# Kernel optimization log

Measured on AMD Instinct MI355X. Metric: run time of the kernel, lower is better.

## Reference

```python
import jax, jax.numpy as jnp
import numpy as np

K = 20          # neighbors per centroid
OUT_CH = 256    # out_channel
EPS = 1e-5      # batchnorm eps


def _bn(x, gamma, beta, axes):
    # batch-norm in training mode (batch statistics), per-channel on last axis
    mu = jnp.mean(x, axis=axes, keepdims=True)
    var = jnp.var(x, axis=axes, keepdims=True)
    return (x - mu) * jax.lax.rsqrt(var + EPS) * gamma + beta


def _forward(centroid, xyz, radius, dist,
             w_xyz, b_xyz, g0, be0, w1, g1, be1, w2, g2, be2):
    B, N, _ = xyz.shape
    M = centroid.shape[1]
    # --- sample_and_group: radius mask + index sort + gather ---
    ar = jnp.arange(N, dtype=jnp.int32)                       # [N]
    idx = jnp.where(dist > radius, N, ar[None, None, :])      # [B,M,N]
    idx = jnp.sort(idx, axis=-1)[:, :, :K]                    # [B,M,K] lowest in-radius indices
    first = idx[:, :, :1]
    idx = jnp.where(idx == N, first, idx)                     # pad with first neighbor
    pf = jax.vmap(lambda f, i: f[i])(xyz, idx)                # [B,M,K,3] gather
    # --- concat (points, neighbors, variance) -> 9 channels ---
    pts = jnp.broadcast_to(centroid[:, :, None, :], (B, M, K, 3))
    feat = jnp.concatenate([pts, pf, pf - pts], axis=-1)      # [B,M,K,9]
    # --- 1x1 conv2d + BN2d + GELU (exact erf, as torch nn.GELU) ---
    h = jnp.einsum('bmkc,oc->bmko', feat, w_xyz) + b_xyz      # [B,M,K,C/8]
    h = jax.nn.gelu(_bn(h, g0, be0, axes=(0, 1, 2)), approximate=False)
    # --- max over k neighbors ---
    h = jnp.max(h, axis=2)                                    # [B,M,C/8]
    # --- MLP: Conv1x1 (no bias) + BN1d + GELU, then Conv1x1 + BN1d ---
    h = jnp.einsum('bmc,oc->bmo', h, w1)
    h = jax.nn.gelu(_bn(h, g1, be1, axes=(0, 1)), approximate=False)
    h = jnp.einsum('bmc,oc->bmo', h, w2)
    h = _bn(h, g2, be2, axes=(0, 1))                          # [B,M,OUT_CH]
    return h


def setup_inputs() -> dict:
    key = jax.random.key(0)
    ks = jax.random.split(key, 10)
    B, M, N = 4, 2048, 8192
    c8, c4 = OUT_CH // 8, OUT_CH // 4
    return {
        'centroid': jax.random.uniform(ks[0], (B, M, 3), jnp.float32),
        'xyz': jax.random.uniform(ks[1], (B, N, 3), jnp.float32),
        'radius': jax.random.uniform(ks[2], (B, M, 1), jnp.float32),
        'dist': jax.random.uniform(ks[3], (B, M, N), jnp.float32),
        'w_xyz': jax.random.normal(ks[4], (c8, 9), jnp.float32) * 0.3,
        'b_xyz': jnp.zeros((c8,), jnp.float32),
        'g0': jnp.ones((c8,), jnp.float32),
        'be0': jnp.zeros((c8,), jnp.float32),
        'w1': jax.random.normal(ks[5], (c4, c8), jnp.float32) * 0.2,
        'g1': jnp.ones((c4,), jnp.float32),
        'be1': jnp.zeros((c4,), jnp.float32),
        'w2': jax.random.normal(ks[6], (OUT_CH, c4), jnp.float32) * 0.15,
        'g2': jnp.ones((OUT_CH,), jnp.float32),
        'be2': jnp.zeros((OUT_CH,), jnp.float32),
    }


def reference(centroid, xyz, radius, dist, w_xyz, b_xyz, g0, be0,
              w1, g1, be1, w2, g2, be2):
    return _forward(centroid, xyz, radius, dist, w_xyz, b_xyz, g0, be0,
                    w1, g1, be1, w2, g2, be2)
```

## Files before the change

### kernel.cpp

```cpp
#include <hip/hip_runtime.h>
#include <cstdint>
#include <cstddef>

#define K_NB   20
#define N_PTS  8192
#define C8     32
#define C4     64
#define COUT   256
#define EPSV   1e-5f
#define NROWS  8192
#define NBLK   1024
#define RPW    2
#define NP0    32
#define NP1    32
#define NP2    32

__device__ __forceinline__ float gelu_exact(float x) {
    return 0.5f * x * (1.0f + erff(x * 0.7071067811865476f));
}

__device__ __forceinline__ void grid_barrier(unsigned* __restrict__ arrive,
                                             unsigned* __restrict__ release,
                                             unsigned tag) {
    __syncthreads();
    if (blockIdx.x == 0) {
        for (int i = threadIdx.x; i < NBLK; i += 256) {
            if (i != 0)
                while (__hip_atomic_load(&arrive[i], __ATOMIC_RELAXED,
                                         __HIP_MEMORY_SCOPE_AGENT) != tag)
                    __builtin_amdgcn_s_sleep(1);
        }
        __syncthreads();
        if (threadIdx.x == 0)
            __hip_atomic_store(&release[tag], tag, __ATOMIC_RELEASE,
                               __HIP_MEMORY_SCOPE_AGENT);
    } else {
        if (threadIdx.x == 0) {
            __hip_atomic_store(&arrive[blockIdx.x], tag, __ATOMIC_RELEASE,
                               __HIP_MEMORY_SCOPE_AGENT);
            while (__hip_atomic_load(&release[tag], __ATOMIC_RELAXED,
                                     __HIP_MEMORY_SCOPE_AGENT) != tag)
                __builtin_amdgcn_s_sleep(1);
        }
        __syncthreads();
    }
}

__device__ __forceinline__ double agent_load(const double* p) {
    return __hip_atomic_load(p, __ATOMIC_RELAXED, __HIP_MEMORY_SCOPE_AGENT);
}

__device__ __forceinline__ int chunk_process(const float4* v, float rad, int base,
                                             int lane, int* __restrict__ idxp, int cnt) {
    #pragma unroll
    for (int s = 0; s < 4; s++) {
        unsigned mloc = (v[s].x <= rad ? 1u : 0u) | (v[s].y <= rad ? 2u : 0u)
                      | (v[s].z <= rad ? 4u : 0u) | (v[s].w <= rad ? 8u : 0u);
        uint64_t b0 = __ballot(mloc & 1u);
        uint64_t b1 = __ballot(mloc & 2u);
        uint64_t b2 = __ballot(mloc & 4u);
        uint64_t b3 = __ballot(mloc & 8u);
        uint64_t lt = (1ull << lane) - 1ull;
        int r = __popcll(b0 & lt) + __popcll(b1 & lt)
              + __popcll(b2 & lt) + __popcll(b3 & lt);
        const int myidx = base + s * 256 + lane * 4;
        if (mloc & 1u) { int p = cnt + r; if (p < K_NB) idxp[p] = myidx + 0; r++; }
        if (mloc & 2u) { int p = cnt + r; if (p < K_NB) idxp[p] = myidx + 1; r++; }
        if (mloc & 4u) { int p = cnt + r; if (p < K_NB) idxp[p] = myidx + 2; r++; }
        if (mloc & 8u) { int p = cnt + r; if (p < K_NB) idxp[p] = myidx + 3; r++; }
        cnt += __popcll(b0) + __popcll(b1) + __popcll(b2) + __popcll(b3);
    }
    return cnt;
}

__global__ __launch_bounds__(256, 4) void k_fused(
    const float* __restrict__ centroid, const float* __restrict__ xyz,
    const float* __restrict__ radius,   const float* __restrict__ dist,
    const float* __restrict__ w_xyz,    const float* __restrict__ b_xyz,
    const float* __restrict__ g0,  const float* __restrict__ be0,
    const float* __restrict__ w1,  const float* __restrict__ g1,
    const float* __restrict__ be1, const float* __restrict__ w2,
    const float* __restrict__ g2,  const float* __restrict__ be2,
    float* __restrict__ out,
    double* __restrict__ p0sum, double* __restrict__ p0sq,
    double* __restrict__ p1sum, double* __restrict__ p1sq,
    double* __restrict__ p2sum, double* __restrict__ p2sq,
    unsigned* __restrict__ barr_arrive, unsigned* __restrict__ barr_release)
{
    __shared__ int   idx_sh[4][RPW][K_NB];
    __shared__ float ss[256], qq[256];
    __shared__ float sc0[C8],  sh0[C8];
    __shared__ float w1t[C8 * C4];
    __shared__ float a_sh[4][RPW][C8];
    __shared__ float sc1[C4],  sh1[C4];
    __shared__ float a1_sh[4][RPW][C4];
    __shared__ float s2s[4][COUT], q2s[4][COUT];
    __shared__ float sc2[COUT], sh2[COUT];

    const int tid  = threadIdx.x;
    const int wave = tid >> 6;
    const int lane = tid & 63;
    const int gw   = blockIdx.x * 4 + wave;
    const int row0 = gw * RPW;
    const int b    = row0 >> 11;
    const int ch   = lane & 31;
    const int kk   = lane >> 5;

    const float* wr = w_xyz + ch * 9;
    const float wc0 = wr[0] - wr[6], wc1 = wr[1] - wr[7], wc2 = wr[2] - wr[8];
    const float wp0 = wr[3] + wr[6], wp1 = wr[4] + wr[7], wp2 = wr[5] + wr[8];
    const float bch = b_xyz[ch];

    const float rad0 = radius[row0];
    const float rad1 = radius[row0 + 1];
    const float* d0 = dist + (size_t)row0 * N_PTS;
    const float* d1 = d0 + N_PTS;
    int* idx0 = idx_sh[wave][0];
    int* idx1 = idx_sh[wave][1];

    float4 va[4], vb[4];
    #pragma unroll
    for (int s = 0; s < 4; s++) va[s] = reinterpret_cast<const float4*>(d0 + s * 256)[lane];
    #pragma unroll
    for (int s = 0; s < 4; s++) vb[s] = reinterpret_cast<const float4*>(d1 + s * 256)[lane];
    int cnt0 = chunk_process(va, rad0, 0, lane, idx0, 0);
    int cnt1 = chunk_process(vb, rad1, 0, lane, idx1, 0);
    for (int base = 1024; base < N_PTS && cnt0 < K_NB; base += 1024) {
        #pragma unroll
        for (int s = 0; s < 4; s++)
            va[s] = reinterpret_cast<const float4*>(d0 + base + s * 256)[lane];
        cnt0 = chunk_process(va, rad0, base, lane, idx0, cnt0);
    }
    for (int base = 1024; base < N_PTS && cnt1 < K_NB; base += 1024) {
        #pragma unroll
        for (int s = 0; s < 4; s++)
            vb[s] = reinterpret_cast<const float4*>(d1 + base + s * 256)[lane];
        cnt1 = chunk_process(vb, rad1, base, lane, idx1, cnt1);
    }

    {
        const int cf = (cnt0 < K_NB) ? cnt0 : K_NB;
        const int fv = (cnt0 == 0) ? (N_PTS - 1) : idx0[0];
        if (lane < K_NB && lane >= cf) idx0[lane] = fv;
    }
    {
        const int cf = (cnt1 < K_NB) ? cnt1 : K_NB;
        const int fv = (cnt1 == 0) ? (N_PTS - 1) : idx1[0];
        if (lane < K_NB && lane >= cf) idx1[lane] = fv;
    }

    float e[RPW];
    float s_acc = 0.f, q_acc = 0.f;
    #pragma unroll
    for (int r = 0; r < RPW; ++r) {
        const int row = row0 + r;
        const float cterm = bch + centroid[row * 3 + 0] * wc0
                          + centroid[row * 3 + 1] * wc1
                          + centroid[row * 3 + 2] * wc2;
        const int* idxp = idx_sh[wave][r];
        float s = 0.f, q = 0.f, mn = 3.0e38f, mx = -3.0e38f;
        #pragma unroll
        for (int t = 0; t < 10; t++) {
            const int idx = idxp[2 * t + kk];
            const float* p = xyz + ((size_t)b * N_PTS + idx) * 3;
            const float h = cterm + p[0] * wp0 + p[1] * wp1 + p[2] * wp2;
            s += h; q += h * h;
            mn = fminf(mn, h); mx = fmaxf(mx, h);
        }
        s_acc += s; q_acc += q;
        mn = fminf(mn, __shfl_xor(mn, 32));
        mx = fmaxf(mx, __shfl_xor(mx, 32));
        e[r] = (lane < 32) ? mn : mx;
    }

    for (int i = tid; i < C4 * C8; i += 256) {
        const int o = i >> 5, c = i & 31;
        w1t[c * C4 + o] = w1[i];
    }

    ss[tid] = s_acc; qq[tid] = q_acc;
    __syncthreads();
    if (tid < C8) {
        float S = 0.f, Q = 0.f;
        #pragma unroll
        for (int rr = 0; rr < 8; rr++) { S += ss[tid + 32 * rr]; Q += qq[tid + 32 * rr]; }
        const int part = blockIdx.x & (NP0 - 1);
        atomicAdd(&p0sum[part * C8 + tid], (double)S);
        atomicAdd(&p0sq [part * C8 + tid], (double)Q);
    }
    grid_barrier(barr_arrive, barr_release, 1u);

    if (tid < C8) {
        double S = 0.0, Q = 0.0;
        #pragma unroll 8
        for (int p = 0; p < NP0; p++) { S += agent_load(&p0sum[p * C8 + tid]);
                                        Q += agent_load(&p0sq [p * C8 + tid]); }
        const double inv = 1.0 / (double)((long)NROWS * K_NB);
        const double mu  = S * inv;
        const double var = Q * inv - mu * mu;
        const float sf = g0[tid] / sqrtf((float)var + EPSV);
        sc0[tid] = sf;
        sh0[tid] = be0[tid] - (float)mu * sf;
    }
    __syncthreads();

    float h1r[RPW];
    #pragma unroll
    for (int r = 0; r < RPW; ++r) {
        float g = gelu_exact(e[r] * sc0[ch] + sh0[ch]);
        g = fmaxf(g, __shfl_xor(g, 32));
        if (lane < 32) a_sh[wave][r][lane] = g;
    }
    #pragma unroll
    for (int r = 0; r < RPW; ++r) {
        float acc = 0.f;
        #pragma unroll
        for (int c = 0; c < C8; c++) acc += a_sh[wave][r][c] * w1t[c * C4 + lane];
        h1r[r] = acc;
    }
    ss[tid] = h1r[0] + h1r[1];
    qq[tid] = h1r[0] * h1r[0] + h1r[1] * h1r[1];
    __syncthreads();
    if (tid < C4) {
        const float S = ss[tid] + ss[tid + 64] + ss[tid + 128] + ss[tid + 192];
        const float Q = qq[tid] + qq[tid + 64] + qq[tid + 128] + qq[tid + 192];
        const int part = blockIdx.x & (NP1 - 1);
        atomicAdd(&p1sum[part * C4 + tid], (double)S);
        atomicAdd(&p1sq [part * C4 + tid], (double)Q);
    }
    grid_barrier(barr_arrive, barr_release, 2u);

    if (tid < C4) {
        double S = 0.0, Q = 0.0;
        #pragma unroll 8
        for (int p = 0; p < NP1; p++) { S += agent_load(&p1sum[p * C4 + tid]);
                                        Q += agent_load(&p1sq [p * C4 + tid]); }
        const double inv = 1.0 / (double)NROWS;
        const double mu  = S * inv;
        const double var = Q * inv - mu * mu;
        const float sf = g1[tid] / sqrtf((float)var + EPSV);
        sc1[tid] = sf;
        sh1[tid] = be1[tid] - (float)mu * sf;
    }
    __syncthreads();
    #pragma unroll
    for (int r = 0; r < RPW; ++r)
        a1_sh[wave][r][lane] = gelu_exact(h1r[r] * sc1[lane] + sh1[lane]);

    const float4* w2v = reinterpret_cast<const float4*>(w2);
    float acc[RPW][4] = {};
    #pragma unroll
    for (int j = 0; j < 4; j++) {
        const int o = j * 64 + lane;
        #pragma unroll
        for (int c4 = 0; c4 < 16; c4++) {
            const float4 wv = w2v[o * 16 + c4];
            #pragma unroll
            for (int r = 0; r < RPW; r++) {
                acc[r][j] += a1_sh[wave][r][4 * c4 + 0] * wv.x
                           + a1_sh[wave][r][4 * c4 + 1] * wv.y
                           + a1_sh[wave][r][4 * c4 + 2] * wv.z
                           + a1_sh[wave][r][4 * c4 + 3] * wv.w;
            }
        }
    }
    #pragma unroll
    for (int j = 0; j < 4; j++) {
        float S = 0.f, Q = 0.f;
        #pragma unroll
        for (int r = 0; r < RPW; ++r) { S += acc[r][j]; Q += acc[r][j] * acc[r][j]; }
        s2s[wave][j * 64 + lane] = S;
        q2s[wave][j * 64 + lane] = Q;
    }
    __syncthreads();
    {
        const float S = s2s[0][tid] + s2s[1][tid] + s2s[2][tid] + s2s[3][tid];
        const float Q = q2s[0][tid] + q2s[1][tid] + q2s[2][tid] + q2s[3][tid];
        const int part = blockIdx.x & (NP2 - 1);
        atomicAdd(&p2sum[part * COUT + tid], (double)S);
        atomicAdd(&p2sq [part * COUT + tid], (double)Q);
    }
    grid_barrier(barr_arrive, barr_release, 3u);

    {
        double S = 0.0, Q = 0.0;
        #pragma unroll 8
        for (int p = 0; p < NP2; p++) { S += agent_load(&p2sum[p * COUT + tid]);
                                        Q += agent_load(&p2sq [p * COUT + tid]); }
        const double inv = 1.0 / (double)NROWS;
        const double mu  = S * inv;
        const double var = Q * inv - mu * mu;
        const float sf = g2[tid] / sqrtf((float)var + EPSV);
        sc2[tid] = sf;
        sh2[tid] = be2[tid] - (float)mu * sf;
    }
    __syncthreads();
    #pragma unroll
    for (int r = 0; r < RPW; ++r) {
        float* orow = out + (size_t)(row0 + r) * COUT;
        #pragma unroll
        for (int j = 0; j < 4; j++) {
            const int oc = j * 64 + lane;
            orow[oc] = acc[r][j] * sc2[oc] + sh2[oc];
        }
    }
}

extern "C" void kernel_launch(void* const* d_in, const int* in_sizes, int n_in,
                              void* d_out, int out_size, void* d_ws, size_t ws_size,
                              hipStream_t stream) {
    const float* centroid = (const float*)d_in[0];
    const float* xyz      = (const float*)d_in[1];
    const float* radius   = (const float*)d_in[2];
    const float* dist     = (const float*)d_in[3];
    const float* w_xyz    = (const float*)d_in[4];
    const float* b_xyz    = (const float*)d_in[5];
    const float* g0       = (const float*)d_in[6];
    const float* be0      = (const float*)d_in[7];
    const float* w1       = (const float*)d_in[8];
    const float* g1       = (const float*)d_in[9];
    const float* be1      = (const float*)d_in[10];
    const float* w2       = (const float*)d_in[11];
    const float* g2       = (const float*)d_in[12];
    const float* be2      = (const float*)d_in[13];
    float* out = (float*)d_out;

    char* ws = (char*)d_ws;
    double* p0sum = (double*)ws;
    double* p0sq  = p0sum + NP0 * C8;
    double* p1sum = p0sq  + NP0 * C8;
    double* p1sq  = p1sum + NP1 * C4;
    double* p2sum = p1sq  + NP1 * C4;
    double* p2sq  = p2sum + NP2 * COUT;
    unsigned* barr_arrive  = (unsigned*)(ws + 262144);
    unsigned* barr_release = (unsigned*)(ws + 262144 + 8192);

    k_fused<<<NBLK, 256, 0, stream>>>(centroid, xyz, radius, dist,
                                      w_xyz, b_xyz, g0, be0, w1, g1, be1,
                                      w2, g2, be2, out,
                                      p0sum, p0sq, p1sum, p1sq, p2sum, p2sq,
                                      barr_arrive, barr_release);
}
```

Before: 437.8 us.

## Process one row per wave, double grid size, and shard barrier release flags

Each wave now handles a single row instead of two, which doubles the block count to 2048 and raises launch bounds to 8 blocks per CU. Shared memory is packed into one aliased buffer so the extra blocks fit. The grid barrier's release flag is spread across 64 slots so waiting blocks poll different addresses instead of all polling one. This trades some per-row latency hiding, since two rows' dist scans no longer overlap in one wave, for more resident waves, and the barrier now has to check twice as many arrivals.

```diff
diff --git a/kernel.cpp b/kernel.cpp
--- a/kernel.cpp
+++ b/kernel.cpp
@@ -9,8 +9,7 @@
 #define COUT   256
 #define EPSV   1e-5f
 #define NROWS  8192
-#define NBLK   1024
-#define RPW    2
+#define NBLK   2048
 #define NP0    32
 #define NP1    32
 #define NP2    32
@@ -31,14 +30,15 @@
                     __builtin_amdgcn_s_sleep(1);
         }
         __syncthreads();
-        if (threadIdx.x == 0)
-            __hip_atomic_store(&release[tag], tag, __ATOMIC_RELEASE,
-                               __HIP_MEMORY_SCOPE_AGENT);
+        if (threadIdx.x < 64)
+            __hip_atomic_store(&release[tag * 64 + threadIdx.x], tag,
+                               __ATOMIC_RELEASE, __HIP_MEMORY_SCOPE_AGENT);
     } else {
         if (threadIdx.x == 0) {
             __hip_atomic_store(&arrive[blockIdx.x], tag, __ATOMIC_RELEASE,
                                __HIP_MEMORY_SCOPE_AGENT);
-            while (__hip_atomic_load(&release[tag], __ATOMIC_RELAXED,
+            while (__hip_atomic_load(&release[tag * 64 + (blockIdx.x & 63)],
+                                     __ATOMIC_RELAXED,
                                      __HIP_MEMORY_SCOPE_AGENT) != tag)
                 __builtin_amdgcn_s_sleep(1);
         }
@@ -73,7 +73,21 @@
     return cnt;
 }
 
-__global__ __launch_bounds__(256, 4) void k_fused(
+#define SM_SS    0
+#define SM_QQ    1024
+#define SM_U     2048
+#define SM_SC0   10240
+#define SM_SH0   10368
+#define SM_ASH   10496
+#define SM_SC1   11008
+#define SM_SH1   11264
+#define SM_A1    11520
+#define SM_SC2   12544
+#define SM_SH2   13568
+#define SM_IDX   14592
+#define SM_SIZE  14976
+
+__global__ __launch_bounds__(256, 8) void k_fused(
     const float* __restrict__ centroid, const float* __restrict__ xyz,
     const float* __restrict__ radius,   const float* __restrict__ dist,
     const float* __restrict__ w_xyz,    const float* __restrict__ b_xyz,
@@ -87,98 +101,78 @@
     double* __restrict__ p2sum, double* __restrict__ p2sq,
     unsigned* __restrict__ barr_arrive, unsigned* __restrict__ barr_release)
 {
-    __shared__ int   idx_sh[4][RPW][K_NB];
-    __shared__ float ss[256], qq[256];
-    __shared__ float sc0[C8],  sh0[C8];
-    __shared__ float w1t[C8 * C4];
-    __shared__ float a_sh[4][RPW][C8];
-    __shared__ float sc1[C4],  sh1[C4];
-    __shared__ float a1_sh[4][RPW][C4];
-    __shared__ float s2s[4][COUT], q2s[4][COUT];
-    __shared__ float sc2[COUT], sh2[COUT];
+    __shared__ __align__(16) char smem[SM_SIZE];
+    float* ss  = (float*)(smem + SM_SS);
+    float* qq  = (float*)(smem + SM_QQ);
+    float* sc0 = (float*)(smem + SM_SC0);
+    float* sh0 = (float*)(smem + SM_SH0);
+    float* sc1 = (float*)(smem + SM_SC1);
+    float* sh1 = (float*)(smem + SM_SH1);
+    float* sc2 = (float*)(smem + SM_SC2);
+    float* sh2 = (float*)(smem + SM_SH2);
 
     const int tid  = threadIdx.x;
     const int wave = tid >> 6;
     const int lane = tid & 63;
-    const int gw   = blockIdx.x * 4 + wave;
-    const int row0 = gw * RPW;
-    const int b    = row0 >> 11;
+    const int row  = blockIdx.x * 4 + wave;
+    const int b    = row >> 11;
     const int ch   = lane & 31;
     const int kk   = lane >> 5;
+
+    float* a_shw = (float*)(smem + SM_ASH) + wave * C8;
+    float* a1w   = (float*)(smem + SM_A1)  + wave * C4;
+    int*   idxp  = (int*)  (smem + SM_IDX) + wave * K_NB;
 
     const float* wr = w_xyz + ch * 9;
     const float wc0 = wr[0] - wr[6], wc1 = wr[1] - wr[7], wc2 = wr[2] - wr[8];
     const float wp0 = wr[3] + wr[6], wp1 = wr[4] + wr[7], wp2 = wr[5] + wr[8];
     const float bch = b_xyz[ch];
 
-    const float rad0 = radius[row0];
-    const float rad1 = radius[row0 + 1];
-    const float* d0 = dist + (size_t)row0 * N_PTS;
-    const float* d1 = d0 + N_PTS;
-    int* idx0 = idx_sh[wave][0];
-    int* idx1 = idx_sh[wave][1];
-
-    float4 va[4], vb[4];
+    const float rad = radius[row];
+    const float* drow = dist + (size_t)row * N_PTS;
+
+    float4 va[4];
     #pragma unroll
-    for (int s = 0; s < 4; s++) va[s] = reinterpret_cast<const float4*>(d0 + s * 256)[lane];
+    for (int s = 0; s < 4; s++)
+        va[s] = reinterpret_cast<const float4*>(drow + s * 256)[lane];
+    int cnt = chunk_process(va, rad, 0, lane, idxp, 0);
+    for (int base = 1024; base < N_PTS && cnt < K_NB; base += 1024) {
+        #pragma unroll
+        for (int s = 0; s < 4; s++)
+            va[s] = reinterpret_cast<const float4*>(drow + base + s * 256)[lane];
+        cnt = chunk_process(va, rad, base, lane, idxp, cnt);
+    }
+    {
+        const int cf = (cnt < K_NB) ? cnt : K_NB;
+        const int fv = (cnt == 0) ? (N_PTS - 1) : idxp[0];
+        if (lane < K_NB && lane >= cf) idxp[lane] = fv;
+    }
+
+    const float cterm = bch + centroid[row * 3 + 0] * wc0
+                      + centroid[row * 3 + 1] * wc1
+                      + centroid[row * 3 + 2] * wc2;
+    float s = 0.f, q = 0.f, mn = 3.0e38f, mx = -3.0e38f;
     #pragma unroll
-    for (int s = 0; s < 4; s++) vb[s] = reinterpret_cast<const float4*>(d1 + s * 256)[lane];
-    int cnt0 = chunk_process(va, rad0, 0, lane, idx0, 0);
-    int cnt1 = chunk_process(vb, rad1, 0, lane, idx1, 0);
-    for (int base = 1024; base < N_PTS && cnt0 < K_NB; base += 1024) {
-        #pragma unroll
-        for (int s = 0; s < 4; s++)
-            va[s] = reinterpret_cast<const float4*>(d0 + base + s * 256)[lane];
-        cnt0 = chunk_process(va, rad0, base, lane, idx0, cnt0);
-    }
-    for (int base = 1024; base < N_PTS && cnt1 < K_NB; base += 1024) {
-        #pragma unroll
-        for (int s = 0; s < 4; s++)
-            vb[s] = reinterpret_cast<const float4*>(d1 + base + s * 256)[lane];
-        cnt1 = chunk_process(vb, rad1, base, lane, idx1, cnt1);
-    }
-
-    {
-        const int cf = (cnt0 < K_NB) ? cnt0 : K_NB;
-        const int fv = (cnt0 == 0) ? (N_PTS - 1) : idx0[0];
-        if (lane < K_NB && lane >= cf) idx0[lane] = fv;
-    }
-    {
-        const int cf = (cnt1 < K_NB) ? cnt1 : K_NB;
-        const int fv = (cnt1 == 0) ? (N_PTS - 1) : idx1[0];
-        if (lane < K_NB && lane >= cf) idx1[lane] = fv;
-    }
-
-    float e[RPW];
-    float s_acc = 0.f, q_acc = 0.f;
-    #pragma unroll
-    for (int r = 0; r < RPW; ++r) {
-        const int row = row0 + r;
-        const float cterm = bch + centroid[row * 3 + 0] * wc0
-                          + centroid[row * 3 + 1] * wc1
-                          + centroid[row * 3 + 2] * wc2;
-        const int* idxp = idx_sh[wave][r];
-        float s = 0.f, q = 0.f, mn = 3.0e38f, mx = -3.0e38f;
-        #pragma unroll
-        for (int t = 0; t < 10; t++) {
-            const int idx = idxp[2 * t + kk];
-            const float* p = xyz + ((size_t)b * N_PTS + idx) * 3;
-            const float h = cterm + p[0] * wp0 + p[1] * wp1 + p[2] * wp2;
-            s += h; q += h * h;
-            mn = fminf(mn, h); mx = fmaxf(mx, h);
-        }
-        s_acc += s; q_acc += q;
-        mn = fminf(mn, __shfl_xor(mn, 32));
-        mx = fmaxf(mx, __shfl_xor(mx, 32));
-        e[r] = (lane < 32) ? mn : mx;
-    }
-
-    for (int i = tid; i < C4 * C8; i += 256) {
-        const int o = i >> 5, c = i & 31;
-        w1t[c * C4 + o] = w1[i];
-    }
-
-    ss[tid] = s_acc; qq[tid] = q_acc;
+    for (int t = 0; t < 10; t++) {
+        const int idx = idxp[2 * t + kk];
+        const float* p = xyz + ((size_t)b * N_PTS + idx) * 3;
+        const float h = cterm + p[0] * wp0 + p[1] * wp1 + p[2] * wp2;
+        s += h; q += h * h;
+        mn = fminf(mn, h); mx = fmaxf(mx, h);
+    }
+    mn = fminf(mn, __shfl_xor(mn, 32));
+    mx = fmaxf(mx, __shfl_xor(mx, 32));
+    const float e = (lane < 32) ? mn : mx;
+
+    {
+        float* w1t = (float*)(smem + SM_U);
+        for (int i = tid; i < C4 * C8; i += 256) {
+            const int o = i >> 5, c = i & 31;
+            w1t[c * C4 + o] = w1[i];
+        }
+    }
+
+    ss[tid] = s; qq[tid] = q;
     __syncthreads();
     if (tid < C8) {
         float S = 0.f, Q = 0.f;
@@ -204,22 +198,18 @@
     }
     __syncthreads();
 
-    float h1r[RPW];
-    #pragma unroll
-    for (int r = 0; r < RPW; ++r) {
-        float g = gelu_exact(e[r] * sc0[ch] + sh0[ch]);
+    {
+        float g = gelu_exact(e * sc0[ch] + sh0[ch]);
         g = fmaxf(g, __shfl_xor(g, 32));
-        if (lane < 32) a_sh[wave][r][lane] = g;
-    }
-    #pragma unroll
-    for (int r = 0; r < RPW; ++r) {
-        float acc = 0.f;
-        #pragma unroll
-        for (int c = 0; c < C8; c++) acc += a_sh[wave][r][c] * w1t[c * C4 + lane];
-        h1r[r] = acc;
-    }
-    ss[tid] = h1r[0] + h1r[1];
-    qq[tid] = h1r[0] * h1r[0] + h1r[1] * h1r[1];
+        if (lane < 32) a_shw[lane] = g;
+    }
+    float h1r = 0.f;
+    {
+        const float* w1t = (const float*)(smem + SM_U);
+        #pragma unroll
+        for (int c = 0; c < C8; c++) h1r += a_shw[c] * w1t[c * C4 + lane];
+    }
+    ss[tid] = h1r; qq[tid] = h1r * h1r;
     __syncthreads();
     if (tid < C4) {
         const float S = ss[tid] + ss[tid + 64] + ss[tid + 128] + ss[tid + 192];
@@ -243,39 +233,32 @@
         sh1[tid] = be1[tid] - (float)mu * sf;
     }
     __syncthreads();
-    #pragma unroll
-    for (int r = 0; r < RPW; ++r)
-        a1_sh[wave][r][lane] = gelu_exact(h1r[r] * sc1[lane] + sh1[lane]);
+    a1w[lane] = gelu_exact(h1r * sc1[lane] + sh1[lane]);
 
     const float4* w2v = reinterpret_cast<const float4*>(w2);
-    float acc[RPW][4] = {};
+    const float4* a1v = reinterpret_cast<const float4*>(a1w);
+    float acc[4] = {};
     #pragma unroll
     for (int j = 0; j < 4; j++) {
         const int o = j * 64 + lane;
         #pragma unroll
         for (int c4 = 0; c4 < 16; c4++) {
             const float4 wv = w2v[o * 16 + c4];
-            #pragma unroll
-            for (int r = 0; r < RPW; r++) {
-                acc[r][j] += a1_sh[wave][r][4 * c4 + 0] * wv.x
-                           + a1_sh[wave][r][4 * c4 + 1] * wv.y
-                           + a1_sh[wave][r][4 * c4 + 2] * wv.z
-                           + a1_sh[wave][r][4 * c4 + 3] * wv.w;
-            }
-        }
-    }
-    #pragma unroll
-    for (int j = 0; j < 4; j++) {
-        float S = 0.f, Q = 0.f;
-        #pragma unroll
-        for (int r = 0; r < RPW; ++r) { S += acc[r][j]; Q += acc[r][j] * acc[r][j]; }
-        s2s[wave][j * 64 + lane] = S;
-        q2s[wave][j * 64 + lane] = Q;
-    }
-    __syncthreads();
-    {
-        const float S = s2s[0][tid] + s2s[1][tid] + s2s[2][tid] + s2s[3][tid];
-        const float Q = q2s[0][tid] + q2s[1][tid] + q2s[2][tid] + q2s[3][tid];
+            const float4 av = a1v[c4];
+            acc[j] += av.x * wv.x + av.y * wv.y + av.z * wv.z + av.w * wv.w;
+        }
+    }
+    {
+        float* s2s = (float*)(smem + SM_U);
+        float* q2s = s2s + 4 * COUT;
+        #pragma unroll
+        for (int j = 0; j < 4; j++) {
+            s2s[wave * COUT + j * 64 + lane] = acc[j];
+            q2s[wave * COUT + j * 64 + lane] = acc[j] * acc[j];
+        }
+        __syncthreads();
+        const float S = s2s[tid] + s2s[COUT + tid] + s2s[2 * COUT + tid] + s2s[3 * COUT + tid];
+        const float Q = q2s[tid] + q2s[COUT + tid] + q2s[2 * COUT + tid] + q2s[3 * COUT + tid];
         const int part = blockIdx.x & (NP2 - 1);
         atomicAdd(&p2sum[part * COUT + tid], (double)S);
         atomicAdd(&p2sq [part * COUT + tid], (double)Q);
@@ -295,13 +278,12 @@
         sh2[tid] = be2[tid] - (float)mu * sf;
     }
     __syncthreads();
-    #pragma unroll
-    for (int r = 0; r < RPW; ++r) {
-        float* orow = out + (size_t)(row0 + r) * COUT;
+    {
+        float* orow = out + (size_t)row * COUT;
         #pragma unroll
         for (int j = 0; j < 4; j++) {
             const int oc = j * 64 + lane;
-            orow[oc] = acc[r][j] * sc2[oc] + sh2[oc];
+            orow[oc] = acc[j] * sc2[oc] + sh2[oc];
         }
     }
 }
@@ -333,7 +315,7 @@
     double* p2sum = p1sq  + NP1 * C4;
     double* p2sq  = p2sum + NP2 * COUT;
     unsigned* barr_arrive  = (unsigned*)(ws + 262144);
-    unsigned* barr_release = (unsigned*)(ws + 262144 + 8192);
+    unsigned* barr_release = (unsigned*)(ws + 262144 + 16384);
 
     k_fused<<<NBLK, 256, 0, stream>>>(centroid, xyz, radius, dist,
                                       w_xyz, b_xyz, g0, be0, w1, g1, be1,
```

New measurement: 553.0 us. 26.3% more time.
